# Kernel optimization log

Measured on AMD Instinct MI355X. Metric: run time of the kernel, lower is better.

The kernel has to match this reference:

```python
import jax, jax.numpy as jnp
import numpy as np

TOKENS, D_IN, D_OUT = 8192, 4096, 4096

def setup_inputs() -> dict:
    key = jax.random.key(0)
    k1, k2, k3 = jax.random.split(key, 3)
    x = jax.random.normal(k1, (TOKENS, D_IN), dtype=jnp.float32)
    # original init: uniform(-1, 1) on weights of shape [out, in]
    w_pos = jax.random.uniform(k2, (D_OUT, D_IN), dtype=jnp.float32, minval=-1.0, maxval=1.0)
    w_neg = jax.random.uniform(k3, (D_OUT, D_IN), dtype=jnp.float32, minval=-1.0, maxval=1.0)
    return {"x": x, "w_pos": w_pos, "w_neg": w_neg}

def _ste_binarize(w):
    # (w > 0).float() in fwd, identity grad (STE): stop_grad(bin - w) + w
    b = (w > 0).astype(w.dtype)
    return jax.lax.stop_gradient(b - w) + w

def reference(x, w_pos, w_neg):
    tern_pos = _ste_binarize(w_pos)  # [O, I]
    tern_neg = _ste_binarize(w_neg)  # [O, I]
    # y = x @ tern_pos^T - x @ tern_neg^T  (biases unused in original forward)
    y = jnp.einsum('ti,oi->to', x, tern_pos) - jnp.einsum('ti,oi->to', x, tern_neg)
    return y
```

## Files before the change

kernel.cpp:

```cpp
#include <hip/hip_runtime.h>
#include <stdint.h>


#define TOKENS 8192
#define DIN    4096
#define DOUT   4096

typedef __bf16  bf16x8  __attribute__((ext_vector_type(8)));
typedef float   floatx4 __attribute__((ext_vector_type(4)));

__device__ __forceinline__ void async_copy16(const void* g, void* l) {
  __builtin_amdgcn_global_load_lds(
      (const __attribute__((address_space(1))) void*)g,
      (__attribute__((address_space(3))) void*)l, 16, 0, 0);
}

__device__ __forceinline__ unsigned short f2bf_rne(float f) {
  union { float f; uint32_t u; } v; v.f = f;
  uint32_t u = v.u;
  u += 0x7fffu + ((u >> 16) & 1u);
  return (unsigned short)(u >> 16);
}

__device__ __forceinline__ unsigned short tern_bits(float p, float n) {
  bool bp = p > 0.0f, bn = n > 0.0f;
  return (unsigned short)(bp == bn ? 0u : (bp ? 0x3f80u : 0xbf80u));
}

__global__ __launch_bounds__(256) void cvt_x_kernel(
    const float4* __restrict__ x, ushort4* __restrict__ xb) {
  const uint32_t stride = gridDim.x * blockDim.x;
  uint32_t i = blockIdx.x * blockDim.x + threadIdx.x;
#pragma unroll
  for (int it = 0; it < 4; ++it, i += stride) {
    float4 v = x[i];
    ushort4 o;
    o.x = f2bf_rne(v.x); o.y = f2bf_rne(v.y);
    o.z = f2bf_rne(v.z); o.w = f2bf_rne(v.w);
    xb[i] = o;
  }
}

__global__ __launch_bounds__(256) void tern_kernel(
    const float4* __restrict__ wp, const float4* __restrict__ wn,
    ushort4* __restrict__ t) {
  const uint32_t stride = gridDim.x * blockDim.x;
  uint32_t i = blockIdx.x * blockDim.x + threadIdx.x;
#pragma unroll
  for (int it = 0; it < 4; ++it, i += stride) {
    float4 p = wp[i];
    float4 n = wn[i];
    ushort4 o;
    o.x = tern_bits(p.x, n.x);
    o.y = tern_bits(p.y, n.y);
    o.z = tern_bits(p.z, n.z);
    o.w = tern_bits(p.w, n.w);
    t[i] = o;
  }
}


#define LDS_BUF   65536u
#define LDS_B_OFF 32768u
#define LDS_KC    16384u

__global__ __launch_bounds__(512, 2) void gemm_bt(
    const unsigned short* __restrict__ A,
    const unsigned short* __restrict__ B,
    float* __restrict__ C)
{
  __shared__ __align__(16) char lds[131072];

  const int tid   = threadIdx.x;
  const int lane  = tid & 63;
  const int wid   = tid >> 6;
  const int waveM = wid >> 2;
  const int waveN = wid & 3;

  const uint32_t flat = blockIdx.x;
  const uint32_t swz  = ((flat & 7u) << 6) | (flat >> 3);
  const uint32_t bm = (swz >> 4) * 256u;
  const uint32_t bn = (swz & 15u) * 256u;

  const uint32_t srow  = (uint32_t)(tid >> 6) * 32u + (uint32_t)((tid & 63) >> 2);
  const uint32_t slot  = (uint32_t)(tid & 3);
  const uint32_t chnk  = slot ^ ((srow >> 1) & 3u);
  const uint32_t stA   = (bm + srow) * (DIN * 2u) + chnk * 16u;
  const uint32_t stB   = (bn + srow) * (DIN * 2u) + chnk * 16u;
  const uint32_t ldsSt = (uint32_t)(tid >> 6) * 2048u + (uint32_t)(tid & 63) * 16u;
  const char* Ab = (const char*)A;
  const char* Bb = (const char*)B;

  const int mrow = lane & 15;
  const int q    = lane >> 4;
  const int xs   = (q ^ ((mrow >> 1) & 3)) * 16;
  const uint32_t aFragBase = (uint32_t)waveM * 8192u + (uint32_t)mrow * 64u + (uint32_t)xs;
  const uint32_t bFragBase = LDS_B_OFF + (uint32_t)waveN * 4096u
                           + (uint32_t)mrow * 64u + (uint32_t)xs;

  floatx4 acc[8][4];
#pragma unroll
  for (int m = 0; m < 8; ++m)
#pragma unroll
    for (int n = 0; n < 4; ++n)
      acc[m][n] = (floatx4)0.0f;

  bf16x8 a[4], b[4];

#define STAGE_A(BUF, KH, KB) do {                                          \
    uint32_t g_ = stA + (KB) + (KH) * 64u;                                 \
    uint32_t l_ = (BUF) * LDS_BUF + (KH) * LDS_KC + ldsSt;                 \
    async_copy16(Ab + g_,           lds + l_);                             \
    async_copy16(Ab + g_ + 131072u, lds + l_ + 1024u);                     \
  } while (0)

#define STAGE_B(BUF, KH, KB) do {                                          \
    uint32_t g_ = stB + (KB) + (KH) * 64u;                                 \
    uint32_t l_ = (BUF) * LDS_BUF + LDS_B_OFF + (KH) * LDS_KC + ldsSt;     \
    async_copy16(Bb + g_,           lds + l_);                             \
    async_copy16(Bb + g_ + 131072u, lds + l_ + 1024u);                     \
  } while (0)

#define PHASE(BUF, KC, MH, STAGE_STMT) do {                                \
    if ((MH) == 0) {                                                       \
      _Pragma("unroll")                                                    \
      for (int n_ = 0; n_ < 4; ++n_)                                       \
        b[n_] = *(const bf16x8*)(lds + (BUF) * LDS_BUF + (KC) * LDS_KC     \
                                 + (uint32_t)n_ * 1024u + bFragBase);      \
      _Pragma("unroll")                                                    \
      for (int m_ = 0; m_ < 4; ++m_)                                       \
        a[m_] = *(const bf16x8*)(lds + (BUF) * LDS_BUF + (KC) * LDS_KC     \
                                 + (uint32_t)m_ * 1024u + aFragBase);      \
    } else {                                                               \
      _Pragma("unroll")                                                    \
      for (int m_ = 0; m_ < 4; ++m_)                                       \
        a[m_] = *(const bf16x8*)(lds + (BUF) * LDS_BUF + (KC) * LDS_KC     \
                                 + (uint32_t)(m_ + 4) * 1024u + aFragBase);\
    }                                                                      \
    STAGE_STMT;                                                            \
    __builtin_amdgcn_s_barrier();                                          \
    asm volatile("s_waitcnt lgkmcnt(0)" ::: "memory");                     \
    __builtin_amdgcn_sched_barrier(0);                                     \
    __builtin_amdgcn_s_setprio(1);                                         \
    _Pragma("unroll")                                                      \
    for (int m_ = 0; m_ < 4; ++m_)                                         \
      _Pragma("unroll")                                                    \
      for (int n_ = 0; n_ < 4; ++n_)                                       \
        acc[(MH) * 4 + m_][n_] = __builtin_amdgcn_mfma_f32_16x16x32_bf16(  \
            a[m_], b[n_], acc[(MH) * 4 + m_][n_], 0, 0, 0);                \
    __builtin_amdgcn_s_setprio(0);                                         \
  } while (0)

#define VM6 asm volatile("s_waitcnt vmcnt(6)" ::: "memory")
#define BAR __builtin_amdgcn_s_barrier()

  STAGE_B(0, 0, 0u);   STAGE_A(0, 0, 0u);
  STAGE_B(0, 1, 0u);   STAGE_A(0, 1, 0u);
  STAGE_B(1, 0, 128u); STAGE_A(1, 0, 128u);
  STAGE_B(1, 1, 128u);
  VM6;
  BAR;

#pragma unroll 1
  for (int i = 0; i < 32; ++i) {
    const uint32_t kb1 = (uint32_t)(2 * i + 1) * 128u;
    const uint32_t kb2 = (uint32_t)((2 * i + 2) & 63) * 128u;
    const uint32_t kb3 = (uint32_t)((2 * i + 3) & 63) * 128u;

    PHASE(0, 0, 0, STAGE_A(1, 1, kb1));        BAR;
    PHASE(0, 0, 1, STAGE_B(0, 0, kb2));        BAR;
    PHASE(0, 1, 0, STAGE_A(0, 0, kb2));        BAR;
    PHASE(0, 1, 1, STAGE_B(0, 1, kb2));  VM6;  BAR;
    PHASE(1, 0, 0, STAGE_A(0, 1, kb2));        BAR;
    PHASE(1, 0, 1, STAGE_B(1, 0, kb3));        BAR;
    PHASE(1, 1, 0, STAGE_A(1, 0, kb3));        BAR;
    PHASE(1, 1, 1, STAGE_B(1, 1, kb3));  VM6;  BAR;
  }

  const int col0 = (int)bn + waveN * 64 + (lane & 15);
  const int row0 = (int)bm + waveM * 128 + (lane >> 4) * 4;
  float* Cp = C + (size_t)row0 * DOUT + col0;
#pragma unroll
  for (int m = 0; m < 8; ++m)
#pragma unroll
    for (int n = 0; n < 4; ++n)
#pragma unroll
      for (int r = 0; r < 4; ++r)
        Cp[(size_t)(m * 16 + r) * DOUT + n * 16] = acc[m][n][r];

#undef STAGE_A
#undef STAGE_B
#undef PHASE
#undef VM6
#undef BAR
}

extern "C" void kernel_launch(void* const* d_in, const int* in_sizes, int n_in,
                              void* d_out, int out_size, void* d_ws, size_t ws_size,
                              hipStream_t stream) {
  const float* x  = (const float*)d_in[0];
  const float* wp = (const float*)d_in[1];
  const float* wn = (const float*)d_in[2];
  float* out = (float*)d_out;

  unsigned short* xb   = (unsigned short*)d_ws;
  unsigned short* tern = xb + (size_t)TOKENS * DIN;

  cvt_x_kernel<<<TOKENS * DIN / 4 / 4 / 256, 256, 0, stream>>>(
      (const float4*)x, (ushort4*)xb);
  tern_kernel<<<DOUT * DIN / 4 / 4 / 256, 256, 0, stream>>>(
      (const float4*)wp, (const float4*)wn, (ushort4*)tern);

  gemm_bt<<<TOKENS / 256 * (DOUT / 256), 512, 0, stream>>>(xb, tern, out);
}
```

Baseline: 536.3 us.

## Double-buffer LDS fragment registers and fuse prep kernels into one launch

The GEMM main loop now keeps two register sets for the A and B fragments. The next phase's LDS reads are issued before the current phase's MFMAs, so LDS latency overlaps with matrix math instead of stalling before each phase. Barrier and vmcnt wait placement is reworked to match, using vmcnt(8) or no wait on alternating phases. Separately, the x-to-bf16 conversion and the ternary weight build are merged into one prep kernel to save a launch. The extra fragment registers raise VGPR pressure, and the changed wait counts could create a race between async LDS fills and the fragment reads if they are miscounted.

```diff
diff --git a/kernel.cpp b/kernel.cpp
--- a/kernel.cpp
+++ b/kernel.cpp
@@ -27,35 +27,36 @@
   return (unsigned short)(bp == bn ? 0u : (bp ? 0x3f80u : 0xbf80u));
 }
 
-__global__ __launch_bounds__(256) void cvt_x_kernel(
-    const float4* __restrict__ x, ushort4* __restrict__ xb) {
-  const uint32_t stride = gridDim.x * blockDim.x;
-  uint32_t i = blockIdx.x * blockDim.x + threadIdx.x;
-#pragma unroll
-  for (int it = 0; it < 4; ++it, i += stride) {
-    float4 v = x[i];
-    ushort4 o;
-    o.x = f2bf_rne(v.x); o.y = f2bf_rne(v.y);
-    o.z = f2bf_rne(v.z); o.w = f2bf_rne(v.w);
-    xb[i] = o;
-  }
-}
-
-__global__ __launch_bounds__(256) void tern_kernel(
+__global__ __launch_bounds__(256) void prep_kernel(
+    const float4* __restrict__ x, ushort4* __restrict__ xb,
     const float4* __restrict__ wp, const float4* __restrict__ wn,
     ushort4* __restrict__ t) {
-  const uint32_t stride = gridDim.x * blockDim.x;
-  uint32_t i = blockIdx.x * blockDim.x + threadIdx.x;
-#pragma unroll
-  for (int it = 0; it < 4; ++it, i += stride) {
-    float4 p = wp[i];
-    float4 n = wn[i];
-    ushort4 o;
-    o.x = tern_bits(p.x, n.x);
-    o.y = tern_bits(p.y, n.y);
-    o.z = tern_bits(p.z, n.z);
-    o.w = tern_bits(p.w, n.w);
-    t[i] = o;
+  const uint32_t bid = blockIdx.x;
+  if (bid < 8192u) {
+    const uint32_t stride = 8192u * 256u;
+    uint32_t i = bid * 256u + threadIdx.x;
+#pragma unroll
+    for (int it = 0; it < 4; ++it, i += stride) {
+      float4 v = x[i];
+      ushort4 o;
+      o.x = f2bf_rne(v.x); o.y = f2bf_rne(v.y);
+      o.z = f2bf_rne(v.z); o.w = f2bf_rne(v.w);
+      xb[i] = o;
+    }
+  } else {
+    const uint32_t stride = 4096u * 256u;
+    uint32_t i = (bid - 8192u) * 256u + threadIdx.x;
+#pragma unroll
+    for (int it = 0; it < 4; ++it, i += stride) {
+      float4 p = wp[i];
+      float4 n = wn[i];
+      ushort4 o;
+      o.x = tern_bits(p.x, n.x);
+      o.y = tern_bits(p.y, n.y);
+      o.z = tern_bits(p.z, n.z);
+      o.w = tern_bits(p.w, n.w);
+      t[i] = o;
+    }
   }
 }
 
@@ -105,7 +106,7 @@
     for (int n = 0; n < 4; ++n)
       acc[m][n] = (floatx4)0.0f;
 
-  bf16x8 a[4], b[4];
+  bf16x8 a0[4], a1[4], b0[4], b1[4];
 
 #define STAGE_A(BUF, KH, KB) do {                                          \
     uint32_t g_ = stA + (KB) + (KH) * 64u;                                 \
@@ -121,25 +122,28 @@
     async_copy16(Bb + g_ + 131072u, lds + l_ + 1024u);                     \
   } while (0)
 
-#define PHASE(BUF, KC, MH, STAGE_STMT) do {                                \
-    if ((MH) == 0) {                                                       \
-      _Pragma("unroll")                                                    \
-      for (int n_ = 0; n_ < 4; ++n_)                                       \
-        b[n_] = *(const bf16x8*)(lds + (BUF) * LDS_BUF + (KC) * LDS_KC     \
+#define IA(DST, BUF, KC, MH) do {                                          \
+    _Pragma("unroll")                                                      \
+    for (int m_ = 0; m_ < 4; ++m_)                                         \
+      DST[m_] = *(const bf16x8*)(lds + (BUF) * LDS_BUF + (KC) * LDS_KC     \
+                                 + (uint32_t)(m_ + (MH) * 4) * 1024u       \
+                                 + aFragBase);                             \
+  } while (0)
+
+#define IB(DST, BUF, KC) do {                                              \
+    _Pragma("unroll")                                                      \
+    for (int n_ = 0; n_ < 4; ++n_)                                         \
+      DST[n_] = *(const bf16x8*)(lds + (BUF) * LDS_BUF + (KC) * LDS_KC     \
                                  + (uint32_t)n_ * 1024u + bFragBase);      \
-      _Pragma("unroll")                                                    \
-      for (int m_ = 0; m_ < 4; ++m_)                                       \
-        a[m_] = *(const bf16x8*)(lds + (BUF) * LDS_BUF + (KC) * LDS_KC     \
-                                 + (uint32_t)m_ * 1024u + aFragBase);      \
-    } else {                                                               \
-      _Pragma("unroll")                                                    \
-      for (int m_ = 0; m_ < 4; ++m_)                                       \
-        a[m_] = *(const bf16x8*)(lds + (BUF) * LDS_BUF + (KC) * LDS_KC     \
-                                 + (uint32_t)(m_ + 4) * 1024u + aFragBase);\
-    }                                                                      \
-    STAGE_STMT;                                                            \
-    __builtin_amdgcn_s_barrier();                                          \
+  } while (0)
+
+#define VM8 asm volatile("s_waitcnt vmcnt(8)" ::: "memory")
+#define NOPW ((void)0)
+
+#define PHASE(MH, AV, BV, ISSUE_STMT, STAGE_STMT, VMW) do {                \
     asm volatile("s_waitcnt lgkmcnt(0)" ::: "memory");                     \
+    __builtin_amdgcn_sched_barrier(0);                                     \
+    ISSUE_STMT;                                                            \
     __builtin_amdgcn_sched_barrier(0);                                     \
     __builtin_amdgcn_s_setprio(1);                                         \
     _Pragma("unroll")                                                      \
@@ -147,19 +151,20 @@
       _Pragma("unroll")                                                    \
       for (int n_ = 0; n_ < 4; ++n_)                                       \
         acc[(MH) * 4 + m_][n_] = __builtin_amdgcn_mfma_f32_16x16x32_bf16(  \
-            a[m_], b[n_], acc[(MH) * 4 + m_][n_], 0, 0, 0);                \
+            AV[m_], BV[n_], acc[(MH) * 4 + m_][n_], 0, 0, 0);              \
     __builtin_amdgcn_s_setprio(0);                                         \
-  } while (0)
-
-#define VM6 asm volatile("s_waitcnt vmcnt(6)" ::: "memory")
-#define BAR __builtin_amdgcn_s_barrier()
+    STAGE_STMT;                                                            \
+    VMW;                                                                   \
+    __builtin_amdgcn_s_barrier();                                          \
+  } while (0)
 
   STAGE_B(0, 0, 0u);   STAGE_A(0, 0, 0u);
   STAGE_B(0, 1, 0u);   STAGE_A(0, 1, 0u);
   STAGE_B(1, 0, 128u); STAGE_A(1, 0, 128u);
   STAGE_B(1, 1, 128u);
-  VM6;
-  BAR;
+  asm volatile("s_waitcnt vmcnt(10)" ::: "memory");
+  __builtin_amdgcn_s_barrier();
+  IB(b0, 0, 0); IA(a0, 0, 0, 0);
 
 #pragma unroll 1
   for (int i = 0; i < 32; ++i) {
@@ -167,14 +172,14 @@
     const uint32_t kb2 = (uint32_t)((2 * i + 2) & 63) * 128u;
     const uint32_t kb3 = (uint32_t)((2 * i + 3) & 63) * 128u;
 
-    PHASE(0, 0, 0, STAGE_A(1, 1, kb1));        BAR;
-    PHASE(0, 0, 1, STAGE_B(0, 0, kb2));        BAR;
-    PHASE(0, 1, 0, STAGE_A(0, 0, kb2));        BAR;
-    PHASE(0, 1, 1, STAGE_B(0, 1, kb2));  VM6;  BAR;
-    PHASE(1, 0, 0, STAGE_A(0, 1, kb2));        BAR;
-    PHASE(1, 0, 1, STAGE_B(1, 0, kb3));        BAR;
-    PHASE(1, 1, 0, STAGE_A(1, 0, kb3));        BAR;
-    PHASE(1, 1, 1, STAGE_B(1, 1, kb3));  VM6;  BAR;
+    PHASE(0, a0, b0, IA(a1, 0, 0, 1),                  STAGE_A(1, 1, kb1), VM8);
+    PHASE(1, a1, b0, { IB(b1, 0, 1); IA(a0, 0, 1, 0); }, STAGE_B(0, 0, kb2), NOPW);
+    PHASE(0, a0, b1, IA(a1, 0, 1, 1),                  STAGE_A(0, 0, kb2), VM8);
+    PHASE(1, a1, b1, { IB(b0, 1, 0); IA(a0, 1, 0, 0); }, STAGE_B(0, 1, kb2), NOPW);
+    PHASE(0, a0, b0, IA(a1, 1, 0, 1),                  STAGE_A(0, 1, kb2), VM8);
+    PHASE(1, a1, b0, { IB(b1, 1, 1); IA(a0, 1, 1, 0); }, STAGE_B(1, 0, kb3), NOPW);
+    PHASE(0, a0, b1, IA(a1, 1, 1, 1),                  STAGE_A(1, 0, kb3), VM8);
+    PHASE(1, a1, b1, { IB(b0, 0, 0); IA(a0, 0, 0, 0); }, STAGE_B(1, 1, kb3), NOPW);
   }
 
   const int col0 = (int)bn + waveN * 64 + (lane & 15);
@@ -190,9 +195,11 @@
 
 #undef STAGE_A
 #undef STAGE_B
+#undef IA
+#undef IB
+#undef VM8
+#undef NOPW
 #undef PHASE
-#undef VM6
-#undef BAR
 }
 
 extern "C" void kernel_launch(void* const* d_in, const int* in_sizes, int n_in,
@@ -206,9 +213,8 @@
   unsigned short* xb   = (unsigned short*)d_ws;
   unsigned short* tern = xb + (size_t)TOKENS * DIN;
 
-  cvt_x_kernel<<<TOKENS * DIN / 4 / 4 / 256, 256, 0, stream>>>(
-      (const float4*)x, (ushort4*)xb);
-  tern_kernel<<<DOUT * DIN / 4 / 4 / 256, 256, 0, stream>>>(
+  prep_kernel<<<12288, 256, 0, stream>>>(
+      (const float4*)x, (ushort4*)xb,
       (const float4*)wp, (const float4*)wn, (ushort4*)tern);
 
   gemm_bt<<<TOKENS / 256 * (DOUT / 256), 512, 0, stream>>>(xb, tern, out);
```

New measurement: 537.7 us. Within noise of the previous version (+0.2%).
